# Optimization experiments

Measured on AMD Instinct MI355X. Metric: run time of the kernel, lower is better.

Reference implementation:

```python
import jax, jax.numpy as jnp
import numpy as np

VOCAB, EMBED, ENC_DIM, HIDDEN, ATTN = 32000, 512, 512, 1024, 128
SRC_LEN, TGT_LEN = 1024, 512


def setup_inputs() -> dict:
    key = jax.random.key(0)
    ks = jax.random.split(key, 16)
    s = lambda fan_in: 1.0 / np.sqrt(fan_in)
    inp = {
        "encoder_outputs": jax.random.normal(ks[0], (SRC_LEN, ENC_DIM), jnp.float32),
        "initial_h": jax.random.normal(ks[1], (HIDDEN,), jnp.float32),
        "initial_c": jnp.zeros((HIDDEN,), jnp.float32),
        "sos_token": 1,
        "target_seq": jax.random.randint(ks[2], (TGT_LEN,), 0, VOCAB, jnp.int32),
        # parameters
        "emb_table": jax.random.normal(ks[3], (VOCAB, EMBED), jnp.float32),
        "Wa_enc": jax.random.normal(ks[4], (ATTN, ENC_DIM), jnp.float32) * s(ENC_DIM),
        "Wa_h": jax.random.normal(ks[5], (ATTN, HIDDEN), jnp.float32) * s(HIDDEN),
        "v_a": jax.random.normal(ks[6], (ATTN,), jnp.float32) * s(ATTN),
        "W_ih": jax.random.normal(ks[7], (4 * HIDDEN, EMBED + ENC_DIM), jnp.float32) * s(EMBED + ENC_DIM),
        "W_hh": jax.random.normal(ks[8], (4 * HIDDEN, HIDDEN), jnp.float32) * s(HIDDEN),
        "b_ih": jnp.zeros((4 * HIDDEN,), jnp.float32),
        "b_hh": jnp.zeros((4 * HIDDEN,), jnp.float32),
        "W_out": jax.random.normal(ks[9], (VOCAB, HIDDEN), jnp.float32) * s(HIDDEN),
        "b_out": jnp.zeros((VOCAB,), jnp.float32),
    }
    return inp


def reference(encoder_outputs, initial_h, initial_c, sos_token, target_seq,
              emb_table, Wa_enc, Wa_h, v_a, W_ih, W_hh, b_ih, b_hh, W_out, b_out):
    # Teacher forcing with ratio 1.0: input token at step t is target_seq[t-1] (sos at t=0).
    prev_tokens = jnp.concatenate([jnp.array([sos_token], dtype=target_seq.dtype), target_seq[:-1]])
    embedded = emb_table[prev_tokens]                      # (T, E)
    enc_proj = encoder_outputs @ Wa_enc.T                  # (S, A), precomputed once

    def step(carry, emb_t):
        h, c = carry
        # Bahdanau attention: v^T tanh(W_enc e_s + W_h h)
        scores = jnp.tanh(enc_proj + Wa_h @ h) @ v_a       # (S,)
        attn = jax.nn.softmax(scores)                      # (S,)
        context = attn @ encoder_outputs                   # (ENC_DIM,)
        x = jnp.concatenate([emb_t, context])              # (E + ENC_DIM,)
        gates = W_ih @ x + b_ih + W_hh @ h + b_hh          # (4H,) order i,f,g,o
        i, f, g, o = jnp.split(gates, 4)
        c_new = jax.nn.sigmoid(f) * c + jax.nn.sigmoid(i) * jnp.tanh(g)
        h_new = jax.nn.sigmoid(o) * jnp.tanh(c_new)
        logits = W_out @ h_new + b_out                     # (V,)
        return (h_new, c_new), (logits, attn)

    (_, _), (all_logits, all_attn) = jax.lax.scan(step, (initial_h, initial_c), embedded)
    return all_logits, all_attn                            # (T, V), (T, S)
```

## Files before the change

kernel.cpp:

```cpp
#include <hip/hip_runtime.h>
#include <hip/hip_bf16.h>

#define VOCAB 32000
#define EMBED 512
#define ENCD  512
#define HID   1024
#define ATTN  128
#define SRC   1024
#define TGT   512
#define NB    64
#define NT    512
#define CHUNK 64

typedef __hip_bfloat16 bf16;
typedef _Float16 f16;
typedef __attribute__((ext_vector_type(2))) _Float16 f16x2;
typedef __attribute__((ext_vector_type(8))) _Float16 f16x8;
typedef __attribute__((ext_vector_type(8))) short bf16x8v;
typedef __attribute__((ext_vector_type(4))) float f32x4;

#define OFF_TP    0
#define OFF_G     131072
#define OFF_HH    1179648
#define OFF_CC    1704960
#define OFF_WAHPB 1705984
#define OFF_PB    1722368
#define OFF_HBUF  1724416
#define OFF_CTR   1725440
#define OFF_WAHT  1725504
#define OFF_WHH   1791040
#define OFF_VT    3888192

__device__ __forceinline__ float sigm(float x){ return 1.f/(1.f+__expf(-x)); }
__device__ __forceinline__ float tanh_f(float x){
  float ax = fabsf(x);
  float e = __expf(-2.f*ax);
  float r = (1.f - e) / (1.f + e);
  return copysignf(r, x);
}
__device__ __forceinline__ short f2bs(float x){
  union { bf16 h; short s; } u; u.h = __float2bfloat16(x); return u.s;
}
__device__ __forceinline__ bf16x8v cvt8(const float* p){
  float4 a = *reinterpret_cast<const float4*>(p);
  float4 b = *reinterpret_cast<const float4*>(p+4);
  bf16x8v r;
  r[0]=f2bs(a.x); r[1]=f2bs(a.y); r[2]=f2bs(a.z); r[3]=f2bs(a.w);
  r[4]=f2bs(b.x); r[5]=f2bs(b.y); r[6]=f2bs(b.z); r[7]=f2bs(b.w);
  return r;
}
__device__ __forceinline__ float aldf(const float* p){
  return __hip_atomic_load(p, __ATOMIC_RELAXED, __HIP_MEMORY_SCOPE_AGENT);
}
__device__ __forceinline__ void astf(float* p, float v){
  __hip_atomic_store(p, v, __ATOMIC_RELAXED, __HIP_MEMORY_SCOPE_AGENT);
}
__device__ __forceinline__ unsigned aldu(const unsigned* p){
  return __hip_atomic_load(p, __ATOMIC_RELAXED, __HIP_MEMORY_SCOPE_AGENT);
}
__device__ __forceinline__ void astu(unsigned* p, unsigned v){
  __hip_atomic_store(p, v, __ATOMIC_RELAXED, __HIP_MEMORY_SCOPE_AGENT);
}

__global__ void k_encTP(const float* __restrict__ enc, const float* __restrict__ Wa_enc,
                        const float* __restrict__ v_a, unsigned* __restrict__ TP){
  __shared__ float eL[16][ENCD];
  int s0 = blockIdx.x*16, tid = threadIdx.x;
  #pragma unroll
  for (int i=0;i<16;i++){
    int li = tid + i*128;
    int t = li>>7, k4 = li&127;
    *reinterpret_cast<float4*>(&eL[t][k4*4]) =
      *reinterpret_cast<const float4*>(enc + (size_t)(s0+t)*ENCD + k4*4);
  }
  __syncthreads();
  const float* w = Wa_enc + (size_t)tid*ENCD;
  float va = v_a[tid];
  float acc[16];
  #pragma unroll
  for (int t=0;t<16;t++) acc[t]=0.f;
  for (int k4=0;k4<128;k4++){
    float4 wv = *reinterpret_cast<const float4*>(w + k4*4);
    #pragma unroll
    for (int t=0;t<16;t++){
      float4 e4 = *reinterpret_cast<const float4*>(&eL[t][k4*4]);
      acc[t] += wv.x*e4.x + wv.y*e4.y + wv.z*e4.z + wv.w*e4.w;
    }
  }
  #pragma unroll
  for (int t=0;t<16;t++){
    float th = tanh_f(acc[t]);
    th = fminf(0.9995f, fmaxf(-0.9995f, th));
    union { f16x2 h; unsigned u; } cv;
    cv.h = (f16x2){ (f16)th, (f16)(va*th) };
    TP[(size_t)(s0+t)*ATTN + tid] = cv.u;
  }
}

__global__ void k_gbase(const int* __restrict__ sos, const int* __restrict__ tgt,
                        const float* __restrict__ embt, const float* __restrict__ W_ih,
                        const float* __restrict__ b_ih, const float* __restrict__ b_hh,
                        f16* __restrict__ Gp){
  __shared__ float eL[16][EMBED];
  int tid = threadIdx.x;
  int t0 = blockIdx.y*16;
  #pragma unroll
  for (int i=0;i<8;i++){
    int li = tid + i*256;
    int t = li>>7, k4 = li&127;
    int tg = t0 + t;
    int tok = (tg==0) ? sos[0] : tgt[tg-1];
    *reinterpret_cast<float4*>(&eL[t][k4*4]) =
      *reinterpret_cast<const float4*>(embt + (size_t)tok*EMBED + k4*4);
  }
  __syncthreads();
  int r = blockIdx.x*256 + tid;
  int g = r>>10, j = r&1023;
  int prow = (j>>4)*64 + g*16 + (j&15);
  const float* w = W_ih + (size_t)r*(EMBED+ENCD);
  float base = b_ih[r] + b_hh[r];
  float acc[16];
  #pragma unroll
  for (int t=0;t<16;t++) acc[t]=0.f;
  for (int k4=0;k4<128;k4++){
    float4 wv = *reinterpret_cast<const float4*>(w + k4*4);
    #pragma unroll
    for (int t=0;t<16;t++){
      float4 e4 = *reinterpret_cast<const float4*>(&eL[t][k4*4]);
      acc[t] += wv.x*e4.x + wv.y*e4.y + wv.z*e4.z + wv.w*e4.w;
    }
  }
  #pragma unroll
  for (int t=0;t<16;t++) Gp[(size_t)(t0+t)*4096 + prow] = (f16)(acc[t] + base);
}

__global__ void k_cvt_whh(const float* __restrict__ W, f16* __restrict__ out){
  int r = blockIdx.x;
  int g = r >> 10, j = r & 1023;
  int prow = (j>>4)*64 + g*16 + (j&15);
  int k0 = threadIdx.x*8;
  float4 a = *reinterpret_cast<const float4*>(W + (size_t)r*HID + k0);
  float4 c = *reinterpret_cast<const float4*>(W + (size_t)r*HID + k0 + 4);
  f16x8 v = { (f16)a.x,(f16)a.y,(f16)a.z,(f16)a.w,(f16)c.x,(f16)c.y,(f16)c.z,(f16)c.w };
  *reinterpret_cast<f16x8*>(out + (size_t)prow*HID + k0) = v;
}
__global__ void k_cvt_wahT(const float* __restrict__ W, f16* __restrict__ out){
  int b = blockIdx.x, a = threadIdx.x;
  const float* src = W + (size_t)a*HID + b*16;
  float4 v0 = *reinterpret_cast<const float4*>(src);
  float4 v1 = *reinterpret_cast<const float4*>(src+4);
  float4 v2 = *reinterpret_cast<const float4*>(src+8);
  float4 v3 = *reinterpret_cast<const float4*>(src+12);
  f16* dst = out + ((size_t)b*128 + a)*16;
  f16x8 w0 = { (f16)v0.x,(f16)v0.y,(f16)v0.z,(f16)v0.w,(f16)v1.x,(f16)v1.y,(f16)v1.z,(f16)v1.w };
  f16x8 w1 = { (f16)v2.x,(f16)v2.y,(f16)v2.z,(f16)v2.w,(f16)v3.x,(f16)v3.y,(f16)v3.z,(f16)v3.w };
  *reinterpret_cast<f16x8*>(dst)   = w0;
  *reinterpret_cast<f16x8*>(dst+8) = w1;
}

__global__ __launch_bounds__(256) void k_gemmV(const float* __restrict__ W_ih,
                                               const float* __restrict__ enc,
                                               f16* __restrict__ Vt){
  int bn = blockIdx.x, bm = blockIdx.y;
  int tid = threadIdx.x;
  int wid = tid>>6, lane = tid&63;
  int wr = wid>>1, wc = wid&1;
  int rowf = lane&15, kg = lane>>4;
  const int m_base = bm*128 + wr*64;
  const int n_base = bn*128 + wc*64;
  const float* Ap[4];
  #pragma unroll
  for (int mt=0;mt<4;mt++){
    int prow = m_base + mt*16 + rowf;
    int bb = prow>>6, g = (prow>>4)&3, jl = prow&15;
    int r = g*HID + bb*16 + jl;
    Ap[mt] = W_ih + (size_t)r*(EMBED+ENCD) + EMBED + kg*8;
  }
  const float* Bp = enc + (size_t)(n_base + rowf)*ENCD + kg*8;
  f32x4 acc[4][4];
  #pragma unroll
  for (int i=0;i<4;i++)
    #pragma unroll
    for (int jv=0;jv<4;jv++) acc[i][jv] = (f32x4){0.f,0.f,0.f,0.f};
  for (int kk=0; kk<ENCD; kk+=32){
    bf16x8v av[4], bv[4];
    #pragma unroll
    for (int mt=0;mt<4;mt++) av[mt] = cvt8(Ap[mt] + kk);
    #pragma unroll
    for (int nt=0;nt<4;nt++) bv[nt] = cvt8(Bp + (size_t)nt*16*ENCD + kk);
    #pragma unroll
    for (int mt=0;mt<4;mt++)
      #pragma unroll
      for (int nt=0;nt<4;nt++)
        acc[mt][nt] = __builtin_amdgcn_mfma_f32_16x16x32_bf16(av[mt], bv[nt], acc[mt][nt], 0,0,0);
  }
  #pragma unroll
  for (int mt=0;mt<4;mt++){
    #pragma unroll
    for (int nt=0;nt<4;nt++){
      int n = n_base + nt*16 + rowf;
      #pragma unroll
      for (int i=0;i<4;i++){
        int m = m_base + mt*16 + kg*4 + i;
        Vt[(size_t)m*SRC + n] = (f16)acc[mt][nt][i];
      }
    }
  }
}

__global__ void k_prep0(const float* __restrict__ h0, const float* __restrict__ c0,
                        const float* __restrict__ Wa_h,
                        float* __restrict__ Hh, float* __restrict__ Cc,
                        unsigned* __restrict__ hbuf, float* __restrict__ wahpb,
                        unsigned* __restrict__ ctr){
  int b = blockIdx.x, tid = threadIdx.x;
  if (b < 8){ Hh[b*128+tid] = h0[b*128+tid]; Cc[b*128+tid] = c0[b*128+tid]; }
  if (b < 4){
    int i = b*128 + tid;
    union { f16x2 h; unsigned u; } cv;
    cv.h = (f16x2){ (f16)h0[2*i], (f16)h0[2*i+1] };
    hbuf[i] = cv.u;
  }
  if (b == 0 && tid < 3) ctr[tid] = 0u;
  __shared__ float hl[16];
  if (tid < 16) hl[tid] = h0[b*16 + tid];
  __syncthreads();
  const float* wr = Wa_h + (size_t)tid*HID + b*16;
  float acc = 0.f;
  #pragma unroll
  for (int i4=0;i4<4;i4++){
    float4 w4 = *reinterpret_cast<const float4*>(wr + i4*4);
    acc += w4.x*hl[i4*4] + w4.y*hl[i4*4+1] + w4.z*hl[i4*4+2] + w4.w*hl[i4*4+3];
  }
  wahpb[b*128 + tid] = acc;
}

__global__ __launch_bounds__(NT) void k_multi(int t0,
    const unsigned* __restrict__ TP, const f16* __restrict__ WahT,
    const f16* __restrict__ Whh_h, const f16* __restrict__ Vt,
    const f16* __restrict__ Gp, const float* __restrict__ v_a,
    float* __restrict__ Hh, float* __restrict__ Cc,
    float* __restrict__ wahpb, float* __restrict__ pbuf,
    unsigned* __restrict__ hbuf, unsigned* __restrict__ ctr,
    float* __restrict__ Pout)
{
  const int b = blockIdx.x, tid = threadIdx.x;
  __shared__ f16x8 hs8[128];
  __shared__ f16x8 ps8[128];
  __shared__ float2 vwp[128];
  __shared__ float vas[128];
  __shared__ float gacc[64];
  __shared__ float g2[64];
  __shared__ float pown[16];
  __shared__ float hnl[16];
  __shared__ f16x2 hnl2[8];
  __shared__ float wpart[8];
  __shared__ float invs;
  __shared__ float cst[16];

  const int l8 = tid >> 3, q8 = tid & 7;

  if (tid < 16)  cst[tid] = Cc[b*16 + tid];
  if (tid < 128) vas[tid] = v_a[tid];

  for (int k = 0; k < CHUNK; ++k){
    const int t = t0 + k;
    const unsigned base = 64u*(unsigned)t;
    if (tid == 0){
      while (aldu(&ctr[2]) < base) __builtin_amdgcn_s_sleep(1);
    }
    __syncthreads();
    if (tid < 128){
      const unsigned* hp = hbuf + (t&1)*512 + tid*4;
      union { unsigned u[4]; f16x8 v; } cv;
      cv.u[0]=aldu(hp); cv.u[1]=aldu(hp+1); cv.u[2]=aldu(hp+2); cv.u[3]=aldu(hp+3);
      hs8[(tid&15)*8 + (tid>>4)] = cv.v;
    }
    {
      int a = tid >> 2, lane4 = tid & 3;
      const float* wp = wahpb + (t&1)*8192 + lane4*128 + a;
      float acc = 0.f;
      #pragma unroll
      for (int m = 0; m < 16; ++m) acc += aldf(wp + m*512);
      acc += __shfl_xor(acc,1); acc += __shfl_xor(acc,2);
      if (lane4 == 0){
        float tw = tanh_f(acc);
        vwp[a] = make_float2(tw, vas[a]*tw);
      }
    }
    __syncthreads();
    {
      int row = tid >> 5, l5 = tid & 31;
      const f16x8* tp8 = (const f16x8*)((const f16*)TP + ((size_t)(b*16+row)*ATTN + l5*4)*2);
      f16x8 tv = tp8[0];
      float sc = 0.f;
      #pragma unroll
      for (int u = 0; u < 4; ++u){
        float T  = (float)tv[2*u];
        float vT = (float)tv[2*u+1];
        float2 vw = vwp[l5*4 + u];
        float num = vT + vw.y;
        float den = fmaf(T, vw.x, 1.f);
        sc = fmaf(num, __builtin_amdgcn_rcpf(den), sc);
      }
      sc += __shfl_xor(sc,1); sc += __shfl_xor(sc,2); sc += __shfl_xor(sc,4);
      sc += __shfl_xor(sc,8); sc += __shfl_xor(sc,16);
      if (l5 == 0){
        float pv = __expf(sc);
        pown[row] = pv;
        astf(&pbuf[(t&1)*1024 + b*16 + row], pv);
      }
    }
    __syncthreads();
    if (tid == 0)
      __hip_atomic_fetch_add(&ctr[1], 1u, __ATOMIC_RELAXED, __HIP_MEMORY_SCOPE_AGENT);
    {
      const f16x8* wr = (const f16x8*)(Whh_h + (size_t)(b*64 + l8)*HID + q8*128);
      float ga = 0.f;
      #pragma unroll
      for (int i = 0; i < 16; ++i){
        f16x8 wv = wr[i];
        f16x8 hv = hs8[i*8 + q8];
        const f16x2* wp = (const f16x2*)&wv;
        const f16x2* hp = (const f16x2*)&hv;
        ga = __builtin_amdgcn_fdot2(wp[0], hp[0], ga, false);
        ga = __builtin_amdgcn_fdot2(wp[1], hp[1], ga, false);
        ga = __builtin_amdgcn_fdot2(wp[2], hp[2], ga, false);
        ga = __builtin_amdgcn_fdot2(wp[3], hp[3], ga, false);
      }
      ga += __shfl_xor(ga,1); ga += __shfl_xor(ga,2); ga += __shfl_xor(ga,4);
      if (q8 == 0) gacc[l8] = ga;
    }
    if (tid == 0){
      while (aldu(&ctr[1]) < base + 64u) __builtin_amdgcn_s_sleep(1);
    }
    __syncthreads();
    {
      float p0 = aldf(&pbuf[(t&1)*1024 + 2*tid]);
      float p1 = aldf(&pbuf[(t&1)*1024 + 2*tid + 1]);
      float s2 = p0 + p1;
      s2 += __shfl_xor(s2,1); s2 += __shfl_xor(s2,2); s2 += __shfl_xor(s2,4);
      s2 += __shfl_xor(s2,8); s2 += __shfl_xor(s2,16); s2 += __shfl_xor(s2,32);
      if ((tid & 63) == 0) wpart[tid >> 6] = s2;
      __syncthreads();
      if (tid == 0){
        float d = 0.f;
        #pragma unroll
        for (int kk = 0; kk < 8; ++kk) d += wpart[kk];
        invs = 1.f/d;
      }
      __syncthreads();
      float iv = invs;
      int q = tid >> 6, i8 = (tid & 63) >> 2, j = tid & 3;
      ((f16x2*)&ps8[i8*8 + q])[j] = (f16x2){ (f16)(p0*iv), (f16)(p1*iv) };
      if (tid < 16) Pout[(size_t)t*SRC + b*16 + tid] = pown[tid]*iv;
    }
    __syncthreads();
    {
      const f16x8* wr = (const f16x8*)(Vt + (size_t)(b*64 + l8)*SRC + q8*128);
      float acc = 0.f;
      #pragma unroll
      for (int i = 0; i < 16; ++i){
        f16x8 wv = wr[i];
        f16x8 pv = ps8[i*8 + q8];
        const f16x2* wp = (const f16x2*)&wv;
        const f16x2* pp = (const f16x2*)&pv;
        acc = __builtin_amdgcn_fdot2(wp[0], pp[0], acc, false);
        acc = __builtin_amdgcn_fdot2(wp[1], pp[1], acc, false);
        acc = __builtin_amdgcn_fdot2(wp[2], pp[2], acc, false);
        acc = __builtin_amdgcn_fdot2(wp[3], pp[3], acc, false);
      }
      acc += __shfl_xor(acc,1); acc += __shfl_xor(acc,2); acc += __shfl_xor(acc,4);
      if (q8 == 0) g2[l8] = acc + gacc[l8] + (float)Gp[(size_t)t*4096 + b*64 + l8];
    }
    __syncthreads();
    if (tid < 16){
      float gi = g2[tid], gf = g2[16+tid], gg = g2[32+tid], go = g2[48+tid];
      float cn = sigm(gf)*cst[tid] + sigm(gi)*tanh_f(gg);
      float hn = sigm(go)*tanh_f(cn);
      cst[tid] = cn;
      hnl[tid] = hn;
      Hh[(size_t)(t+1)*HID + b*16 + tid] = hn;
    }
    __syncthreads();
    if (tid < 8) hnl2[tid] = (f16x2){ (f16)hnl[2*tid], (f16)hnl[2*tid+1] };
    __syncthreads();
    if (tid < 8){
      union { f16x2 h; unsigned u; } cv;
      cv.h = hnl2[tid];
      astu(&hbuf[((t+1)&1)*512 + b*8 + tid], cv.u);
    } else if (tid >= 128 && tid < 256){
      int a = tid - 128;
      const f16x8* wt = (const f16x8*)(WahT + ((size_t)b*128 + a)*16);
      f16x8 w0 = wt[0], w1 = wt[1];
      const f16x2* wp0 = (const f16x2*)&w0;
      const f16x2* wp1 = (const f16x2*)&w1;
      float acc = 0.f;
      acc = __builtin_amdgcn_fdot2(wp0[0], hnl2[0], acc, false);
      acc = __builtin_amdgcn_fdot2(wp0[1], hnl2[1], acc, false);
      acc = __builtin_amdgcn_fdot2(wp0[2], hnl2[2], acc, false);
      acc = __builtin_amdgcn_fdot2(wp0[3], hnl2[3], acc, false);
      acc = __builtin_amdgcn_fdot2(wp1[0], hnl2[4], acc, false);
      acc = __builtin_amdgcn_fdot2(wp1[1], hnl2[5], acc, false);
      acc = __builtin_amdgcn_fdot2(wp1[2], hnl2[6], acc, false);
      acc = __builtin_amdgcn_fdot2(wp1[3], hnl2[7], acc, false);
      astf(&wahpb[((t+1)&1)*8192 + b*128 + a], acc);
    }
    __syncthreads();
    if (tid == 0)
      __hip_atomic_fetch_add(&ctr[2], 1u, __ATOMIC_RELAXED, __HIP_MEMORY_SCOPE_AGENT);
  }
  if (tid < 16) Cc[b*16 + tid] = cst[tid];
}

__global__ __launch_bounds__(256) void k_gemm(const float* __restrict__ A, const float* __restrict__ B,
                                              const float* __restrict__ bias, float* __restrict__ C){
  int bid = blockIdx.x;
  int tile = (bid & 7)*125 + (bid >> 3);
  int bm = tile & 3, bn = tile >> 2;
  int tid = threadIdx.x;
  int wid = tid>>6, lane = tid&63;
  int wr = wid>>1, wc = wid&1;
  int rowf = lane&15, kg = lane>>4;
  const int m_base = bm*128 + wr*64;
  const int n_base = bn*128 + wc*64;
  const float* Ap = A + (size_t)(m_base + rowf)*HID + kg*8;
  const float* Bp = B + (size_t)(n_base + rowf)*HID + kg*8;
  f32x4 acc[4][4];
  #pragma unroll
  for (int i=0;i<4;i++)
    #pragma unroll
    for (int jv=0;jv<4;jv++) acc[i][jv] = (f32x4){0.f,0.f,0.f,0.f};
  for (int kk=0; kk<HID; kk+=32){
    bf16x8v av[4], bv[4];
    #pragma unroll
    for (int mt=0;mt<4;mt++) av[mt] = cvt8(Ap + (size_t)mt*16*HID + kk);
    #pragma unroll
    for (int nt=0;nt<4;nt++) bv[nt] = cvt8(Bp + (size_t)nt*16*HID + kk);
    #pragma unroll
    for (int mt=0;mt<4;mt++)
      #pragma unroll
      for (int nt=0;nt<4;nt++)
        acc[mt][nt] = __builtin_amdgcn_mfma_f32_16x16x32_bf16(av[mt], bv[nt], acc[mt][nt], 0,0,0);
  }
  #pragma unroll
  for (int mt=0;mt<4;mt++){
    #pragma unroll
    for (int nt=0;nt<4;nt++){
      int n = n_base + nt*16 + rowf;
      float bo = bias[n];
      #pragma unroll
      for (int i=0;i<4;i++){
        int m = m_base + mt*16 + kg*4 + i;
        C[(size_t)m*VOCAB + n] = acc[mt][nt][i] + bo;
      }
    }
  }
}

extern "C" void kernel_launch(void* const* d_in, const int* in_sizes, int n_in,
                              void* d_out, int out_size, void* d_ws, size_t ws_size,
                              hipStream_t stream){
  const float* enc    = (const float*)d_in[0];
  const float* h0     = (const float*)d_in[1];
  const float* c0     = (const float*)d_in[2];
  const int*   sos    = (const int*)d_in[3];
  const int*   tgt    = (const int*)d_in[4];
  const float* embt   = (const float*)d_in[5];
  const float* Wa_enc = (const float*)d_in[6];
  const float* Wa_h   = (const float*)d_in[7];
  const float* v_a    = (const float*)d_in[8];
  const float* W_ih   = (const float*)d_in[9];
  const float* W_hh   = (const float*)d_in[10];
  const float* b_ih   = (const float*)d_in[11];
  const float* b_hh   = (const float*)d_in[12];
  const float* W_out  = (const float*)d_in[13];
  const float* b_out  = (const float*)d_in[14];

  float* ws   = (float*)d_ws;
  unsigned* TP = (unsigned*)(ws + OFF_TP);
  f16*   Gp   = (f16*)(ws + OFF_G);
  float* Hh   = ws + OFF_HH;
  float* Cc   = ws + OFF_CC;
  float* wahpb= ws + OFF_WAHPB;
  float* pbuf = ws + OFF_PB;
  unsigned* hbuf = (unsigned*)(ws + OFF_HBUF);
  unsigned* ctr  = (unsigned*)(ws + OFF_CTR);
  f16*   WahT = (f16*)(ws + OFF_WAHT);
  f16*   Whh_h= (f16*)(ws + OFF_WHH);
  f16*   Vt   = (f16*)(ws + OFF_VT);

  float* out_logits = (float*)d_out;
  float* out_attn   = out_logits + (size_t)TGT*VOCAB;

  k_encTP   <<<64, 128, 0, stream>>>(enc, Wa_enc, v_a, TP);
  k_gbase   <<<dim3(16, 32), 256, 0, stream>>>(sos, tgt, embt, W_ih, b_ih, b_hh, Gp);
  k_cvt_whh <<<4096, 128, 0, stream>>>(W_hh, Whh_h);
  k_cvt_wahT<<<64, 128, 0, stream>>>(Wa_h, WahT);
  k_gemmV   <<<dim3(8, 32), 256, 0, stream>>>(W_ih, enc, Vt);
  k_prep0   <<<64, 128, 0, stream>>>(h0, c0, Wa_h, Hh, Cc, hbuf, wahpb, ctr);

  for (int t0 = 0; t0 < TGT; t0 += CHUNK){
    k_multi<<<NB, NT, 0, stream>>>(t0, TP, WahT, Whh_h, Vt, Gp, v_a,
                                   Hh, Cc, wahpb, pbuf, hbuf, ctr, out_attn);
  }

  k_gemm<<<1000, 256, 0, stream>>>(Hh + HID, W_out, b_out, out_logits);
}
```

Before: 3.753 ms.

## Replace atomic counter barriers with per-block flag slots and single persistent launch

Grid-wide synchronization moves from shared atomic fetch-add counters polled by one thread to per-block slot flags written with plain atomic stores and polled by 64 threads in parallel. The recurrence now runs all steps in a single persistent launch instead of eight chunked launches. Softmax normalization is deferred: unnormalized probabilities feed the context matvec and the scale is applied in the gate combine, which removes two block barriers per step. The aim is less contention on one counter and a shorter serial chain per step, at the cost of relying on all 64 blocks being co-resident for the whole run.

```diff
diff --git a/kernel.cpp b/kernel.cpp
--- a/kernel.cpp
+++ b/kernel.cpp
@@ -10,7 +10,6 @@
 #define TGT   512
 #define NB    64
 #define NT    512
-#define CHUNK 64
 
 typedef __hip_bfloat16 bf16;
 typedef _Float16 f16;
@@ -26,10 +25,10 @@
 #define OFF_WAHPB 1705984
 #define OFF_PB    1722368
 #define OFF_HBUF  1724416
-#define OFF_CTR   1725440
-#define OFF_WAHT  1725504
-#define OFF_WHH   1791040
-#define OFF_VT    3888192
+#define OFF_SLOT  1725440
+#define OFF_WAHT  1725568
+#define OFF_WHH   1791104
+#define OFF_VT    3888256
 
 __device__ __forceinline__ float sigm(float x){ return 1.f/(1.f+__expf(-x)); }
 __device__ __forceinline__ float tanh_f(float x){
@@ -60,6 +59,12 @@
 }
 __device__ __forceinline__ void astu(unsigned* p, unsigned v){
   __hip_atomic_store(p, v, __ATOMIC_RELAXED, __HIP_MEMORY_SCOPE_AGENT);
+}
+__device__ __forceinline__ void waitslot(const unsigned* sl, unsigned tgt, int tid){
+  if (tid < NB){
+    while (aldu(&sl[tid]) < tgt) __builtin_amdgcn_s_sleep(1);
+  }
+  __syncthreads();
 }
 
 __global__ void k_encTP(const float* __restrict__ enc, const float* __restrict__ Wa_enc,
@@ -212,7 +217,7 @@
                         const float* __restrict__ Wa_h,
                         float* __restrict__ Hh, float* __restrict__ Cc,
                         unsigned* __restrict__ hbuf, float* __restrict__ wahpb,
-                        unsigned* __restrict__ ctr){
+                        unsigned* __restrict__ slot){
   int b = blockIdx.x, tid = threadIdx.x;
   if (b < 8){ Hh[b*128+tid] = h0[b*128+tid]; Cc[b*128+tid] = c0[b*128+tid]; }
   if (b < 4){
@@ -221,7 +226,7 @@
     cv.h = (f16x2){ (f16)h0[2*i], (f16)h0[2*i+1] };
     hbuf[i] = cv.u;
   }
-  if (b == 0 && tid < 3) ctr[tid] = 0u;
+  if (b == 0 && tid < 2*NB) slot[tid] = 0u;
   __shared__ float hl[16];
   if (tid < 16) hl[tid] = h0[b*16 + tid];
   __syncthreads();
@@ -235,22 +240,24 @@
   wahpb[b*128 + tid] = acc;
 }
 
-__global__ __launch_bounds__(NT) void k_multi(int t0,
+__global__ __launch_bounds__(NT) void k_multi(int nsteps,
     const unsigned* __restrict__ TP, const f16* __restrict__ WahT,
     const f16* __restrict__ Whh_h, const f16* __restrict__ Vt,
     const f16* __restrict__ Gp, const float* __restrict__ v_a,
     float* __restrict__ Hh, float* __restrict__ Cc,
     float* __restrict__ wahpb, float* __restrict__ pbuf,
-    unsigned* __restrict__ hbuf, unsigned* __restrict__ ctr,
+    unsigned* __restrict__ hbuf, unsigned* __restrict__ slot,
     float* __restrict__ Pout)
 {
   const int b = blockIdx.x, tid = threadIdx.x;
+  unsigned* slh = slot;
+  unsigned* slp = slot + NB;
   __shared__ f16x8 hs8[128];
   __shared__ f16x8 ps8[128];
   __shared__ float2 vwp[128];
   __shared__ float vas[128];
-  __shared__ float gacc[64];
-  __shared__ float g2[64];
+  __shared__ float g2a[64];
+  __shared__ float vp2[64];
   __shared__ float pown[16];
   __shared__ float hnl[16];
   __shared__ f16x2 hnl2[8];
@@ -263,13 +270,9 @@
   if (tid < 16)  cst[tid] = Cc[b*16 + tid];
   if (tid < 128) vas[tid] = v_a[tid];
 
-  for (int k = 0; k < CHUNK; ++k){
-    const int t = t0 + k;
-    const unsigned base = 64u*(unsigned)t;
-    if (tid == 0){
-      while (aldu(&ctr[2]) < base) __builtin_amdgcn_s_sleep(1);
-    }
-    __syncthreads();
+  for (int t = 0; t < nsteps; ++t){
+    const unsigned tg1 = (unsigned)(t + 1);
+    waitslot(slh, (unsigned)t, tid);
     if (tid < 128){
       const unsigned* hp = hbuf + (t&1)*512 + tid*4;
       union { unsigned u[4]; f16x8 v; } cv;
@@ -312,8 +315,7 @@
       }
     }
     __syncthreads();
-    if (tid == 0)
-      __hip_atomic_fetch_add(&ctr[1], 1u, __ATOMIC_RELAXED, __HIP_MEMORY_SCOPE_AGENT);
+    if (tid == 0) astu(&slp[b], tg1);
     {
       const f16x8* wr = (const f16x8*)(Whh_h + (size_t)(b*64 + l8)*HID + q8*128);
       float ga = 0.f;
@@ -329,33 +331,26 @@
         ga = __builtin_amdgcn_fdot2(wp[3], hp[3], ga, false);
       }
       ga += __shfl_xor(ga,1); ga += __shfl_xor(ga,2); ga += __shfl_xor(ga,4);
-      if (q8 == 0) gacc[l8] = ga;
-    }
-    if (tid == 0){
-      while (aldu(&ctr[1]) < base + 64u) __builtin_amdgcn_s_sleep(1);
-    }
-    __syncthreads();
+      if (q8 == 0) g2a[l8] = ga + (float)Gp[(size_t)t*4096 + b*64 + l8];
+    }
+    waitslot(slp, tg1, tid);
     {
       float p0 = aldf(&pbuf[(t&1)*1024 + 2*tid]);
       float p1 = aldf(&pbuf[(t&1)*1024 + 2*tid + 1]);
+      int q = tid >> 6, i8 = (tid & 63) >> 2, j = tid & 3;
+      ((f16x2*)&ps8[i8*8 + q])[j] = (f16x2){ (f16)p0, (f16)p1 };
       float s2 = p0 + p1;
       s2 += __shfl_xor(s2,1); s2 += __shfl_xor(s2,2); s2 += __shfl_xor(s2,4);
       s2 += __shfl_xor(s2,8); s2 += __shfl_xor(s2,16); s2 += __shfl_xor(s2,32);
       if ((tid & 63) == 0) wpart[tid >> 6] = s2;
-      __syncthreads();
-      if (tid == 0){
-        float d = 0.f;
-        #pragma unroll
-        for (int kk = 0; kk < 8; ++kk) d += wpart[kk];
-        invs = 1.f/d;
-      }
-      __syncthreads();
-      float iv = invs;
-      int q = tid >> 6, i8 = (tid & 63) >> 2, j = tid & 3;
-      ((f16x2*)&ps8[i8*8 + q])[j] = (f16x2){ (f16)(p0*iv), (f16)(p1*iv) };
-      if (tid < 16) Pout[(size_t)t*SRC + b*16 + tid] = pown[tid]*iv;
-    }
-    __syncthreads();
+    }
+    __syncthreads();
+    if (tid == 0){
+      float d = 0.f;
+      #pragma unroll
+      for (int kk = 0; kk < 8; ++kk) d += wpart[kk];
+      invs = 1.f/d;
+    }
     {
       const f16x8* wr = (const f16x8*)(Vt + (size_t)(b*64 + l8)*SRC + q8*128);
       float acc = 0.f;
@@ -371,16 +366,22 @@
         acc = __builtin_amdgcn_fdot2(wp[3], pp[3], acc, false);
       }
       acc += __shfl_xor(acc,1); acc += __shfl_xor(acc,2); acc += __shfl_xor(acc,4);
-      if (q8 == 0) g2[l8] = acc + gacc[l8] + (float)Gp[(size_t)t*4096 + b*64 + l8];
+      if (q8 == 0) vp2[l8] = acc;
     }
     __syncthreads();
     if (tid < 16){
-      float gi = g2[tid], gf = g2[16+tid], gg = g2[32+tid], go = g2[48+tid];
+      float iv = invs;
+      float gi = g2a[tid]    + vp2[tid]*iv;
+      float gf = g2a[16+tid] + vp2[16+tid]*iv;
+      float gg = g2a[32+tid] + vp2[32+tid]*iv;
+      float go = g2a[48+tid] + vp2[48+tid]*iv;
       float cn = sigm(gf)*cst[tid] + sigm(gi)*tanh_f(gg);
       float hn = sigm(go)*tanh_f(cn);
       cst[tid] = cn;
       hnl[tid] = hn;
       Hh[(size_t)(t+1)*HID + b*16 + tid] = hn;
+    } else if (tid < 32){
+      Pout[(size_t)t*SRC + b*16 + (tid-16)] = pown[tid-16]*invs;
     }
     __syncthreads();
     if (tid < 8) hnl2[tid] = (f16x2){ (f16)hnl[2*tid], (f16)hnl[2*tid+1] };
@@ -407,8 +408,7 @@
       astf(&wahpb[((t+1)&1)*8192 + b*128 + a], acc);
     }
     __syncthreads();
-    if (tid == 0)
-      __hip_atomic_fetch_add(&ctr[2], 1u, __ATOMIC_RELAXED, __HIP_MEMORY_SCOPE_AGENT);
+    if (tid == 0) astu(&slh[b], tg1);
   }
   if (tid < 16) Cc[b*16 + tid] = cst[tid];
 }
@@ -485,7 +485,7 @@
   float* wahpb= ws + OFF_WAHPB;
   float* pbuf = ws + OFF_PB;
   unsigned* hbuf = (unsigned*)(ws + OFF_HBUF);
-  unsigned* ctr  = (unsigned*)(ws + OFF_CTR);
+  unsigned* slot = (unsigned*)(ws + OFF_SLOT);
   f16*   WahT = (f16*)(ws + OFF_WAHT);
   f16*   Whh_h= (f16*)(ws + OFF_WHH);
   f16*   Vt   = (f16*)(ws + OFF_VT);
@@ -498,12 +498,10 @@
   k_cvt_whh <<<4096, 128, 0, stream>>>(W_hh, Whh_h);
   k_cvt_wahT<<<64, 128, 0, stream>>>(Wa_h, WahT);
   k_gemmV   <<<dim3(8, 32), 256, 0, stream>>>(W_ih, enc, Vt);
-  k_prep0   <<<64, 128, 0, stream>>>(h0, c0, Wa_h, Hh, Cc, hbuf, wahpb, ctr);
-
-  for (int t0 = 0; t0 < TGT; t0 += CHUNK){
-    k_multi<<<NB, NT, 0, stream>>>(t0, TP, WahT, Whh_h, Vt, Gp, v_a,
-                                   Hh, Cc, wahpb, pbuf, hbuf, ctr, out_attn);
-  }
+  k_prep0   <<<64, 128, 0, stream>>>(h0, c0, Wa_h, Hh, Cc, hbuf, wahpb, slot);
+
+  k_multi<<<NB, NT, 0, stream>>>(TGT, TP, WahT, Whh_h, Vt, Gp, v_a,
+                                 Hh, Cc, wahpb, pbuf, hbuf, slot, out_attn);
 
   k_gemm<<<1000, 256, 0, stream>>>(Hh + HID, W_out, b_out, out_logits);
 }
```

Result: slower. 3.879 ms (+3.4%).

## Overlap output-logit GEMM with recurrent chunks using extra worker blocks

Applied to the files above, without the earlier changes.

Adds 63 extra blocks to each recurrent-chunk launch. While the 64 recurrence blocks run the next chunk, these blocks compute output logits for the previous 64 timesteps, streaming W_out rows against fp16-converted hidden states held in shared memory. The final GEMM now covers only the last 128 timesteps. The aim is to hide most of the vocab projection behind the latency-bound recurrence. The risks are contention for bandwidth and compute with the spin-waiting recurrence blocks, a much larger shared-memory footprint that also applies to the recurrence blocks, and a slow scalar FMA inner loop.

```diff
diff --git a/kernel.cpp b/kernel.cpp
--- a/kernel.cpp
+++ b/kernel.cpp
@@ -9,6 +9,7 @@
 #define SRC   1024
 #define TGT   512
 #define NB    64
+#define NBW   127
 #define NT    512
 #define CHUNK 64
 
@@ -242,7 +243,9 @@
     float* __restrict__ Hh, float* __restrict__ Cc,
     float* __restrict__ wahpb, float* __restrict__ pbuf,
     unsigned* __restrict__ hbuf, unsigned* __restrict__ ctr,
-    float* __restrict__ Pout)
+    float* __restrict__ Pout,
+    const float* __restrict__ Wout, const float* __restrict__ bout,
+    float* __restrict__ Clog)
 {
   const int b = blockIdx.x, tid = threadIdx.x;
   __shared__ f16x8 hs8[128];
@@ -257,172 +260,206 @@
   __shared__ float wpart[8];
   __shared__ float invs;
   __shared__ float cst[16];
-
-  const int l8 = tid >> 3, q8 = tid & 7;
-
-  if (tid < 16)  cst[tid] = Cc[b*16 + tid];
-  if (tid < 128) vas[tid] = v_a[tid];
-
-  for (int k = 0; k < CHUNK; ++k){
-    const int t = t0 + k;
-    const unsigned base = 64u*(unsigned)t;
-    if (tid == 0){
-      while (aldu(&ctr[2]) < base) __builtin_amdgcn_s_sleep(1);
+  __shared__ f16x2 hL[16][512];
+
+  if (b < NB){
+    const int l8 = tid >> 3, q8 = tid & 7;
+
+    if (tid < 16)  cst[tid] = Cc[b*16 + tid];
+    if (tid < 128) vas[tid] = v_a[tid];
+
+    for (int k = 0; k < CHUNK; ++k){
+      const int t = t0 + k;
+      const unsigned base = 64u*(unsigned)t;
+      if (tid == 0){
+        while (aldu(&ctr[2]) < base) __builtin_amdgcn_s_sleep(1);
+      }
+      __syncthreads();
+      if (tid < 128){
+        const unsigned* hp = hbuf + (t&1)*512 + tid*4;
+        union { unsigned u[4]; f16x8 v; } cv;
+        cv.u[0]=aldu(hp); cv.u[1]=aldu(hp+1); cv.u[2]=aldu(hp+2); cv.u[3]=aldu(hp+3);
+        hs8[(tid&15)*8 + (tid>>4)] = cv.v;
+      }
+      {
+        int a = tid >> 2, lane4 = tid & 3;
+        const float* wp = wahpb + (t&1)*8192 + lane4*128 + a;
+        float acc = 0.f;
+        #pragma unroll
+        for (int m = 0; m < 16; ++m) acc += aldf(wp + m*512);
+        acc += __shfl_xor(acc,1); acc += __shfl_xor(acc,2);
+        if (lane4 == 0){
+          float tw = tanh_f(acc);
+          vwp[a] = make_float2(tw, vas[a]*tw);
+        }
+      }
+      __syncthreads();
+      {
+        int row = tid >> 5, l5 = tid & 31;
+        const f16x8* tp8 = (const f16x8*)((const f16*)TP + ((size_t)(b*16+row)*ATTN + l5*4)*2);
+        f16x8 tv = tp8[0];
+        float sc = 0.f;
+        #pragma unroll
+        for (int u = 0; u < 4; ++u){
+          float T  = (float)tv[2*u];
+          float vT = (float)tv[2*u+1];
+          float2 vw = vwp[l5*4 + u];
+          float num = vT + vw.y;
+          float den = fmaf(T, vw.x, 1.f);
+          sc = fmaf(num, __builtin_amdgcn_rcpf(den), sc);
+        }
+        sc += __shfl_xor(sc,1); sc += __shfl_xor(sc,2); sc += __shfl_xor(sc,4);
+        sc += __shfl_xor(sc,8); sc += __shfl_xor(sc,16);
+        if (l5 == 0){
+          float pv = __expf(sc);
+          pown[row] = pv;
+          astf(&pbuf[(t&1)*1024 + b*16 + row], pv);
+        }
+      }
+      __syncthreads();
+      if (tid == 0)
+        __hip_atomic_fetch_add(&ctr[1], 1u, __ATOMIC_RELAXED, __HIP_MEMORY_SCOPE_AGENT);
+      {
+        const f16x8* wr = (const f16x8*)(Whh_h + (size_t)(b*64 + l8)*HID + q8*128);
+        float ga = 0.f;
+        #pragma unroll
+        for (int i = 0; i < 16; ++i){
+          f16x8 wv = wr[i];
+          f16x8 hv = hs8[i*8 + q8];
+          const f16x2* wp = (const f16x2*)&wv;
+          const f16x2* hp = (const f16x2*)&hv;
+          ga = __builtin_amdgcn_fdot2(wp[0], hp[0], ga, false);
+          ga = __builtin_amdgcn_fdot2(wp[1], hp[1], ga, false);
+          ga = __builtin_amdgcn_fdot2(wp[2], hp[2], ga, false);
+          ga = __builtin_amdgcn_fdot2(wp[3], hp[3], ga, false);
+        }
+        ga += __shfl_xor(ga,1); ga += __shfl_xor(ga,2); ga += __shfl_xor(ga,4);
+        if (q8 == 0) gacc[l8] = ga;
+      }
+      if (tid == 0){
+        while (aldu(&ctr[1]) < base + 64u) __builtin_amdgcn_s_sleep(1);
+      }
+      __syncthreads();
+      {
+        float p0 = aldf(&pbuf[(t&1)*1024 + 2*tid]);
+        float p1 = aldf(&pbuf[(t&1)*1024 + 2*tid + 1]);
+        float s2 = p0 + p1;
+        s2 += __shfl_xor(s2,1); s2 += __shfl_xor(s2,2); s2 += __shfl_xor(s2,4);
+        s2 += __shfl_xor(s2,8); s2 += __shfl_xor(s2,16); s2 += __shfl_xor(s2,32);
+        if ((tid & 63) == 0) wpart[tid >> 6] = s2;
+        __syncthreads();
+        if (tid == 0){
+          float d = 0.f;
+          #pragma unroll
+          for (int kk = 0; kk < 8; ++kk) d += wpart[kk];
+          invs = 1.f/d;
+        }
+        __syncthreads();
+        float iv = invs;
+        int q = tid >> 6, i8 = (tid & 63) >> 2, j = tid & 3;
+        ((f16x2*)&ps8[i8*8 + q])[j] = (f16x2){ (f16)(p0*iv), (f16)(p1*iv) };
+        if (tid < 16) Pout[(size_t)t*SRC + b*16 + tid] = pown[tid]*iv;
+      }
+      __syncthreads();
+      {
+        const f16x8* wr = (const f16x8*)(Vt + (size_t)(b*64 + l8)*SRC + q8*128);
+        float acc = 0.f;
+        #pragma unroll
+        for (int i = 0; i < 16; ++i){
+          f16x8 wv = wr[i];
+          f16x8 pv = ps8[i*8 + q8];
+          const f16x2* wp = (const f16x2*)&wv;
+          const f16x2* pp = (const f16x2*)&pv;
+          acc = __builtin_amdgcn_fdot2(wp[0], pp[0], acc, false);
+          acc = __builtin_amdgcn_fdot2(wp[1], pp[1], acc, false);
+          acc = __builtin_amdgcn_fdot2(wp[2], pp[2], acc, false);
+          acc = __builtin_amdgcn_fdot2(wp[3], pp[3], acc, false);
+        }
+        acc += __shfl_xor(acc,1); acc += __shfl_xor(acc,2); acc += __shfl_xor(acc,4);
+        if (q8 == 0) g2[l8] = acc + gacc[l8] + (float)Gp[(size_t)t*4096 + b*64 + l8];
+      }
+      __syncthreads();
+      if (tid < 16){
+        float gi = g2[tid], gf = g2[16+tid], gg = g2[32+tid], go = g2[48+tid];
+        float cn = sigm(gf)*cst[tid] + sigm(gi)*tanh_f(gg);
+        float hn = sigm(go)*tanh_f(cn);
+        cst[tid] = cn;
+        hnl[tid] = hn;
+        Hh[(size_t)(t+1)*HID + b*16 + tid] = hn;
+      }
+      __syncthreads();
+      if (tid < 8) hnl2[tid] = (f16x2){ (f16)hnl[2*tid], (f16)hnl[2*tid+1] };
+      __syncthreads();
+      if (tid < 8){
+        union { f16x2 h; unsigned u; } cv;
+        cv.h = hnl2[tid];
+        astu(&hbuf[((t+1)&1)*512 + b*8 + tid], cv.u);
+      } else if (tid >= 128 && tid < 256){
+        int a = tid - 128;
+        const f16x8* wt = (const f16x8*)(WahT + ((size_t)b*128 + a)*16);
+        f16x8 w0 = wt[0], w1 = wt[1];
+        const f16x2* wp0 = (const f16x2*)&w0;
+        const f16x2* wp1 = (const f16x2*)&w1;
+        float acc = 0.f;
+        acc = __builtin_amdgcn_fdot2(wp0[0], hnl2[0], acc, false);
+        acc = __builtin_amdgcn_fdot2(wp0[1], hnl2[1], acc, false);
+        acc = __builtin_amdgcn_fdot2(wp0[2], hnl2[2], acc, false);
+        acc = __builtin_amdgcn_fdot2(wp0[3], hnl2[3], acc, false);
+        acc = __builtin_amdgcn_fdot2(wp1[0], hnl2[4], acc, false);
+        acc = __builtin_amdgcn_fdot2(wp1[1], hnl2[5], acc, false);
+        acc = __builtin_amdgcn_fdot2(wp1[2], hnl2[6], acc, false);
+        acc = __builtin_amdgcn_fdot2(wp1[3], hnl2[7], acc, false);
+        astf(&wahpb[((t+1)&1)*8192 + b*128 + a], acc);
+      }
+      __syncthreads();
+      if (tid == 0)
+        __hip_atomic_fetch_add(&ctr[2], 1u, __ATOMIC_RELAXED, __HIP_MEMORY_SCOPE_AGENT);
     }
-    __syncthreads();
-    if (tid < 128){
-      const unsigned* hp = hbuf + (t&1)*512 + tid*4;
-      union { unsigned u[4]; f16x8 v; } cv;
-      cv.u[0]=aldu(hp); cv.u[1]=aldu(hp+1); cv.u[2]=aldu(hp+2); cv.u[3]=aldu(hp+3);
-      hs8[(tid&15)*8 + (tid>>4)] = cv.v;
+    if (tid < 16) Cc[b*16 + tid] = cst[tid];
+  } else if (t0 > 0){
+    const int r = (b - NB)*512 + tid;
+    const bool act = (r < VOCAB);
+    const float* wrow = act ? (Wout + (size_t)r*HID) : Wout;
+    const float  bo   = act ? bout[r] : 0.f;
+    #pragma unroll 1
+    for (int sb = 0; sb < 4; ++sb){
+      const int tb0 = (t0 - 64) + sb*16;
+      #pragma unroll 1
+      for (int i = 0; i < 16; ++i){
+        float2 hv = *reinterpret_cast<const float2*>(Hh + (size_t)(tb0 + 1 + i)*HID + 2*tid);
+        hL[i][tid] = (f16x2){ (f16)hv.x, (f16)hv.y };
+      }
+      __syncthreads();
+      float acc[16];
+      #pragma unroll
+      for (int tt = 0; tt < 16; ++tt) acc[tt] = 0.f;
+      for (int k2 = 0; k2 < 512; ++k2){
+        float2 w2 = *reinterpret_cast<const float2*>(wrow + 2*k2);
+        #pragma unroll
+        for (int tt = 0; tt < 16; ++tt){
+          f16x2 h2 = hL[tt][k2];
+          acc[tt] = fmaf(w2.x, (float)h2[0], acc[tt]);
+          acc[tt] = fmaf(w2.y, (float)h2[1], acc[tt]);
+        }
+      }
+      if (act){
+        #pragma unroll
+        for (int tt = 0; tt < 16; ++tt)
+          Clog[(size_t)(tb0 + tt)*VOCAB + r] = acc[tt] + bo;
+      }
+      __syncthreads();
     }
-    {
-      int a = tid >> 2, lane4 = tid & 3;
-      const float* wp = wahpb + (t&1)*8192 + lane4*128 + a;
-      float acc = 0.f;
-      #pragma unroll
-      for (int m = 0; m < 16; ++m) acc += aldf(wp + m*512);
-      acc += __shfl_xor(acc,1); acc += __shfl_xor(acc,2);
-      if (lane4 == 0){
-        float tw = tanh_f(acc);
-        vwp[a] = make_float2(tw, vas[a]*tw);
-      }
-    }
-    __syncthreads();
-    {
-      int row = tid >> 5, l5 = tid & 31;
-      const f16x8* tp8 = (const f16x8*)((const f16*)TP + ((size_t)(b*16+row)*ATTN + l5*4)*2);
-      f16x8 tv = tp8[0];
-      float sc = 0.f;
-      #pragma unroll
-      for (int u = 0; u < 4; ++u){
-        float T  = (float)tv[2*u];
-        float vT = (float)tv[2*u+1];
-        float2 vw = vwp[l5*4 + u];
-        float num = vT + vw.y;
-        float den = fmaf(T, vw.x, 1.f);
-        sc = fmaf(num, __builtin_amdgcn_rcpf(den), sc);
-      }
-      sc += __shfl_xor(sc,1); sc += __shfl_xor(sc,2); sc += __shfl_xor(sc,4);
-      sc += __shfl_xor(sc,8); sc += __shfl_xor(sc,16);
-      if (l5 == 0){
-        float pv = __expf(sc);
-        pown[row] = pv;
-        astf(&pbuf[(t&1)*1024 + b*16 + row], pv);
-      }
-    }
-    __syncthreads();
-    if (tid == 0)
-      __hip_atomic_fetch_add(&ctr[1], 1u, __ATOMIC_RELAXED, __HIP_MEMORY_SCOPE_AGENT);
-    {
-      const f16x8* wr = (const f16x8*)(Whh_h + (size_t)(b*64 + l8)*HID + q8*128);
-      float ga = 0.f;
-      #pragma unroll
-      for (int i = 0; i < 16; ++i){
-        f16x8 wv = wr[i];
-        f16x8 hv = hs8[i*8 + q8];
-        const f16x2* wp = (const f16x2*)&wv;
-        const f16x2* hp = (const f16x2*)&hv;
-        ga = __builtin_amdgcn_fdot2(wp[0], hp[0], ga, false);
-        ga = __builtin_amdgcn_fdot2(wp[1], hp[1], ga, false);
-        ga = __builtin_amdgcn_fdot2(wp[2], hp[2], ga, false);
-        ga = __builtin_amdgcn_fdot2(wp[3], hp[3], ga, false);
-      }
-      ga += __shfl_xor(ga,1); ga += __shfl_xor(ga,2); ga += __shfl_xor(ga,4);
-      if (q8 == 0) gacc[l8] = ga;
-    }
-    if (tid == 0){
-      while (aldu(&ctr[1]) < base + 64u) __builtin_amdgcn_s_sleep(1);
-    }
-    __syncthreads();
-    {
-      float p0 = aldf(&pbuf[(t&1)*1024 + 2*tid]);
-      float p1 = aldf(&pbuf[(t&1)*1024 + 2*tid + 1]);
-      float s2 = p0 + p1;
-      s2 += __shfl_xor(s2,1); s2 += __shfl_xor(s2,2); s2 += __shfl_xor(s2,4);
-      s2 += __shfl_xor(s2,8); s2 += __shfl_xor(s2,16); s2 += __shfl_xor(s2,32);
-      if ((tid & 63) == 0) wpart[tid >> 6] = s2;
-      __syncthreads();
-      if (tid == 0){
-        float d = 0.f;
-        #pragma unroll
-        for (int kk = 0; kk < 8; ++kk) d += wpart[kk];
-        invs = 1.f/d;
-      }
-      __syncthreads();
-      float iv = invs;
-      int q = tid >> 6, i8 = (tid & 63) >> 2, j = tid & 3;
-      ((f16x2*)&ps8[i8*8 + q])[j] = (f16x2){ (f16)(p0*iv), (f16)(p1*iv) };
-      if (tid < 16) Pout[(size_t)t*SRC + b*16 + tid] = pown[tid]*iv;
-    }
-    __syncthreads();
-    {
-      const f16x8* wr = (const f16x8*)(Vt + (size_t)(b*64 + l8)*SRC + q8*128);
-      float acc = 0.f;
-      #pragma unroll
-      for (int i = 0; i < 16; ++i){
-        f16x8 wv = wr[i];
-        f16x8 pv = ps8[i*8 + q8];
-        const f16x2* wp = (const f16x2*)&wv;
-        const f16x2* pp = (const f16x2*)&pv;
-        acc = __builtin_amdgcn_fdot2(wp[0], pp[0], acc, false);
-        acc = __builtin_amdgcn_fdot2(wp[1], pp[1], acc, false);
-        acc = __builtin_amdgcn_fdot2(wp[2], pp[2], acc, false);
-        acc = __builtin_amdgcn_fdot2(wp[3], pp[3], acc, false);
-      }
-      acc += __shfl_xor(acc,1); acc += __shfl_xor(acc,2); acc += __shfl_xor(acc,4);
-      if (q8 == 0) g2[l8] = acc + gacc[l8] + (float)Gp[(size_t)t*4096 + b*64 + l8];
-    }
-    __syncthreads();
-    if (tid < 16){
-      float gi = g2[tid], gf = g2[16+tid], gg = g2[32+tid], go = g2[48+tid];
-      float cn = sigm(gf)*cst[tid] + sigm(gi)*tanh_f(gg);
-      float hn = sigm(go)*tanh_f(cn);
-      cst[tid] = cn;
-      hnl[tid] = hn;
-      Hh[(size_t)(t+1)*HID + b*16 + tid] = hn;
-    }
-    __syncthreads();
-    if (tid < 8) hnl2[tid] = (f16x2){ (f16)hnl[2*tid], (f16)hnl[2*tid+1] };
-    __syncthreads();
-    if (tid < 8){
-      union { f16x2 h; unsigned u; } cv;
-      cv.h = hnl2[tid];
-      astu(&hbuf[((t+1)&1)*512 + b*8 + tid], cv.u);
-    } else if (tid >= 128 && tid < 256){
-      int a = tid - 128;
-      const f16x8* wt = (const f16x8*)(WahT + ((size_t)b*128 + a)*16);
-      f16x8 w0 = wt[0], w1 = wt[1];
-      const f16x2* wp0 = (const f16x2*)&w0;
-      const f16x2* wp1 = (const f16x2*)&w1;
-      float acc = 0.f;
-      acc = __builtin_amdgcn_fdot2(wp0[0], hnl2[0], acc, false);
-      acc = __builtin_amdgcn_fdot2(wp0[1], hnl2[1], acc, false);
-      acc = __builtin_amdgcn_fdot2(wp0[2], hnl2[2], acc, false);
-      acc = __builtin_amdgcn_fdot2(wp0[3], hnl2[3], acc, false);
-      acc = __builtin_amdgcn_fdot2(wp1[0], hnl2[4], acc, false);
-      acc = __builtin_amdgcn_fdot2(wp1[1], hnl2[5], acc, false);
-      acc = __builtin_amdgcn_fdot2(wp1[2], hnl2[6], acc, false);
-      acc = __builtin_amdgcn_fdot2(wp1[3], hnl2[7], acc, false);
-      astf(&wahpb[((t+1)&1)*8192 + b*128 + a], acc);
-    }
-    __syncthreads();
-    if (tid == 0)
-      __hip_atomic_fetch_add(&ctr[2], 1u, __ATOMIC_RELAXED, __HIP_MEMORY_SCOPE_AGENT);
-  }
-  if (tid < 16) Cc[b*16 + tid] = cst[tid];
-}
-
-__global__ __launch_bounds__(256) void k_gemm(const float* __restrict__ A, const float* __restrict__ B,
-                                              const float* __restrict__ bias, float* __restrict__ C){
-  int bid = blockIdx.x;
-  int tile = (bid & 7)*125 + (bid >> 3);
-  int bm = tile & 3, bn = tile >> 2;
+  }
+}
+
+__global__ __launch_bounds__(256) void k_gemm1(const float* __restrict__ A, const float* __restrict__ B,
+                                               const float* __restrict__ bias, float* __restrict__ C){
+  int bn = blockIdx.x;
   int tid = threadIdx.x;
   int wid = tid>>6, lane = tid&63;
   int wr = wid>>1, wc = wid&1;
   int rowf = lane&15, kg = lane>>4;
-  const int m_base = bm*128 + wr*64;
+  const int m_base = 384 + wr*64;
   const int n_base = bn*128 + wc*64;
   const float* Ap = A + (size_t)(m_base + rowf)*HID + kg*8;
   const float* Bp = B + (size_t)(n_base + rowf)*HID + kg*8;
@@ -501,9 +538,10 @@
   k_prep0   <<<64, 128, 0, stream>>>(h0, c0, Wa_h, Hh, Cc, hbuf, wahpb, ctr);
 
   for (int t0 = 0; t0 < TGT; t0 += CHUNK){
-    k_multi<<<NB, NT, 0, stream>>>(t0, TP, WahT, Whh_h, Vt, Gp, v_a,
-                                   Hh, Cc, wahpb, pbuf, hbuf, ctr, out_attn);
-  }
-
-  k_gemm<<<1000, 256, 0, stream>>>(Hh + HID, W_out, b_out, out_logits);
-}
+    k_multi<<<NBW, NT, 0, stream>>>(t0, TP, WahT, Whh_h, Vt, Gp, v_a,
+                                    Hh, Cc, wahpb, pbuf, hbuf, ctr, out_attn,
+                                    W_out, b_out, out_logits);
+  }
+
+  k_gemm1<<<250, 256, 0, stream>>>(Hh + HID, W_out, b_out, out_logits);
+}
```

Result: slower. 5.355 ms (+42.7%).
